# Kernel optimization log

Hardware: AMD Instinct MI355X
Metric: run time of the kernel (lower is better)

## Reference

```python
import jax, jax.numpy as jnp
import numpy as np

ANCHORS = np.array([[116.0, 90.0], [156.0, 198.0], [373.0, 326.0]], dtype=np.float32)
NUM_CLASSES = 80
IMG_DIM = 608.0
NA = 3  # num anchors


def setup_inputs() -> dict:
    key = jax.random.key(0)
    # raw head output: [B, nA*(nC+6), G, G]
    x = jax.random.normal(key, (32, NA * (NUM_CLASSES + 6), 76, 76), dtype=jnp.float32)
    return {"x": x}


def reference(x):
    B, _, G, _ = x.shape
    stride = IMG_DIM / G
    # [B, A, G, G, nC+6]
    pred = x.reshape(B, NA, NUM_CLASSES + 6, G, G).transpose(0, 1, 3, 4, 2)
    px = jax.nn.sigmoid(pred[..., 0])
    py = jax.nn.sigmoid(pred[..., 1])
    pw = pred[..., 2]
    ph = pred[..., 3]
    pconf = jax.nn.sigmoid(pred[..., 4])
    pcls = jax.nn.sigmoid(pred[..., 5:])  # nC+1 channels (iou_aware=False path)

    grid_x = jnp.arange(G, dtype=x.dtype)[None, None, None, :]  # varies along last (i) axis
    grid_y = jnp.arange(G, dtype=x.dtype)[None, None, :, None]  # varies along row (j) axis
    scaled_anchors = jnp.asarray(ANCHORS, dtype=x.dtype) / stride
    anchor_w = scaled_anchors[:, 0].reshape(1, NA, 1, 1)
    anchor_h = scaled_anchors[:, 1].reshape(1, NA, 1, 1)

    pred_boxes = jnp.stack(
        [px + grid_x, py + grid_y, jnp.exp(pw) * anchor_w, jnp.exp(ph) * anchor_h],
        axis=-1,
    )  # [B, A, G, G, 4]

    n = NA * G * G
    out = jnp.concatenate(
        [
            pred_boxes.reshape(B, n, 4) * stride,
            pconf.reshape(B, n, 1),
            pcls.reshape(B, n, -1),
        ],
        axis=-1,
    )  # [B, nA*G*G, 4+1+(nC+1)]
    return out
```

## Files before the change

kernel.cpp:

```cpp
#include <hip/hip_runtime.h>
#include <cstdint>


#define GDIM 76
#define SP   (GDIM * GDIM)
#define NCH  86
#define NANC 3
#define TS   64
#define NV   (NCH * TS / 4)

typedef float v4f __attribute__((ext_vector_type(4)));

__global__ __launch_bounds__(256) void yolo_decode_kernel(
    const float* __restrict__ in, float* __restrict__ out) {
    __shared__ __align__(16) float tile[TS * NCH];

    const int tid   = threadIdx.x;
    const int chunk = blockIdx.x;
    const int a     = blockIdx.y;
    const int b     = blockIdx.z;
    const int s0    = chunk * TS;
    const int valid = min(TS, SP - s0);

    const float aw = (a == 0) ? 116.0f : (a == 1) ? 156.0f : 373.0f;
    const float ah = (a == 0) ?  90.0f : (a == 1) ? 198.0f : 326.0f;

    const float* inp = in + ((size_t)(b * (NANC * NCH) + a * NCH)) * SP + s0;

    v4f vbuf[6];
    #pragma unroll
    for (int k = 0; k < 6; ++k) {
        const int idx = tid + (k << 8);
        const int c   = idx >> 4;
        const int s4  = (idx & 15) << 2;
        if (idx < NV && s4 < valid)
            vbuf[k] = *(const v4f*)(inp + (size_t)c * SP + s4);
    }

    #pragma unroll
    for (int k = 0; k < 6; ++k) {
        const int idx = tid + (k << 8);
        const int c   = idx >> 4;
        const int s4  = (idx & 15) << 2;
        if (idx < NV && s4 < valid) {
            v4f v = vbuf[k];
            if (c >= 4) {
                #pragma unroll
                for (int j = 0; j < 4; ++j)
                    v[j] = __builtin_amdgcn_rcpf(1.0f + __expf(-v[j]));
            } else if (c == 0) {
                const int sp_ = s0 + s4;
                #pragma unroll
                for (int j = 0; j < 4; ++j) {
                    const float sg = __builtin_amdgcn_rcpf(1.0f + __expf(-v[j]));
                    v[j] = (sg + (float)((sp_ + j) % GDIM)) * 8.0f;
                }
            } else if (c == 1) {
                const int sp_ = s0 + s4;
                #pragma unroll
                for (int j = 0; j < 4; ++j) {
                    const float sg = __builtin_amdgcn_rcpf(1.0f + __expf(-v[j]));
                    v[j] = (sg + (float)((sp_ + j) / GDIM)) * 8.0f;
                }
            } else {
                const float an = (c == 2) ? aw : ah;
                #pragma unroll
                for (int j = 0; j < 4; ++j)
                    v[j] = __expf(v[j]) * an;
            }
            #pragma unroll
            for (int j = 0; j < 4; ++j)
                tile[(s4 + j) * NCH + c] = v[j];
        }
    }
    __syncthreads();

    v4f* outp = (v4f*)(out + ((size_t)b * (NANC * SP) + (size_t)a * SP + (size_t)s0) * NCH);
    const int nvalid = (valid * NCH) >> 2;
    const v4f* lv = (const v4f*)tile;
    #pragma unroll
    for (int k = 0; k < 6; ++k) {
        const int v = tid + (k << 8);
        if (v < nvalid)
            __builtin_nontemporal_store(lv[v], outp + v);
    }
}

extern "C" void kernel_launch(void* const* d_in, const int* in_sizes, int n_in,
                              void* d_out, int out_size, void* d_ws, size_t ws_size,
                              hipStream_t stream) {
    const float* in = (const float*)d_in[0];
    float* out = (float*)d_out;
    const int B = in_sizes[0] / (NANC * NCH * SP);
    dim3 grid((SP + TS - 1) / TS, NANC, B);
    yolo_decode_kernel<<<grid, 256, 0, stream>>>(in, out);
}
```

Before: 322.5 us.

## Replace LDS transpose with per-thread channel loop writing output rows directly

Removes the shared-memory tile and barrier: each thread handles one spatial location, loads its 86 channels in four register batches, decodes them and writes its 86-float output row with 8-byte stores. This is meant to cut LDS traffic and synchronisation and to allow higher occupancy. In exchange, output stores within a wavefront become strided by the row size instead of contiguous, which risks poor write coalescing, and the nontemporal stores are dropped.

```diff
diff --git a/kernel.cpp b/kernel.cpp
--- a/kernel.cpp
+++ b/kernel.cpp
@@ -6,84 +6,61 @@
 #define SP   (GDIM * GDIM)
 #define NCH  86
 #define NANC 3
-#define TS   64
-#define NV   (NCH * TS / 4)
+#define TPB  256
 
-typedef float v4f __attribute__((ext_vector_type(4)));
+typedef float v2f __attribute__((ext_vector_type(2)));
 
-__global__ __launch_bounds__(256) void yolo_decode_kernel(
+__device__ __forceinline__ float fsig(float x) {
+    return __builtin_amdgcn_rcpf(1.0f + __expf(-x));
+}
+
+template<int C0, int NC>
+__device__ __forceinline__ void decode_pass(
+    const float* __restrict__ inp, float* __restrict__ orow,
+    float gx, float gy, float aw, float ah) {
+    float r[NC];
+    #pragma unroll
+    for (int i = 0; i < NC; ++i)
+        r[i] = inp[(size_t)(C0 + i) * SP];
+    #pragma unroll
+    for (int i = 0; i < NC; ++i) {
+        const int c = C0 + i;
+        const float x = r[i];
+        if      (c == 0) r[i] = (fsig(x) + gx) * 8.0f;
+        else if (c == 1) r[i] = (fsig(x) + gy) * 8.0f;
+        else if (c == 2) r[i] = __expf(x) * aw;
+        else if (c == 3) r[i] = __expf(x) * ah;
+        else             r[i] = fsig(x);
+    }
+    #pragma unroll
+    for (int p = 0; p < NC / 2; ++p) {
+        v2f t;
+        t.x = r[2 * p];
+        t.y = r[2 * p + 1];
+        *(v2f*)(orow + C0 + 2 * p) = t;
+    }
+}
+
+__global__ __launch_bounds__(TPB, 6) void yolo_decode_kernel(
     const float* __restrict__ in, float* __restrict__ out) {
-    __shared__ __align__(16) float tile[TS * NCH];
-
-    const int tid   = threadIdx.x;
-    const int chunk = blockIdx.x;
-    const int a     = blockIdx.y;
-    const int b     = blockIdx.z;
-    const int s0    = chunk * TS;
-    const int valid = min(TS, SP - s0);
+    const int s = blockIdx.x * TPB + threadIdx.x;
+    const int a = blockIdx.y;
+    const int b = blockIdx.z;
+    if (s >= SP) return;
 
     const float aw = (a == 0) ? 116.0f : (a == 1) ? 156.0f : 373.0f;
     const float ah = (a == 0) ?  90.0f : (a == 1) ? 198.0f : 326.0f;
 
-    const float* inp = in + ((size_t)(b * (NANC * NCH) + a * NCH)) * SP + s0;
+    const float* inp = in + (size_t)((b * NANC + a) * NCH) * SP + s;
+    float* orow = out + ((size_t)(b * NANC + a) * SP + (size_t)s) * NCH;
 
-    v4f vbuf[6];
-    #pragma unroll
-    for (int k = 0; k < 6; ++k) {
-        const int idx = tid + (k << 8);
-        const int c   = idx >> 4;
-        const int s4  = (idx & 15) << 2;
-        if (idx < NV && s4 < valid)
-            vbuf[k] = *(const v4f*)(inp + (size_t)c * SP + s4);
-    }
+    const float gx = (float)(s % GDIM);
+    const float gy = (float)(s / GDIM);
 
-    #pragma unroll
-    for (int k = 0; k < 6; ++k) {
-        const int idx = tid + (k << 8);
-        const int c   = idx >> 4;
-        const int s4  = (idx & 15) << 2;
-        if (idx < NV && s4 < valid) {
-            v4f v = vbuf[k];
-            if (c >= 4) {
-                #pragma unroll
-                for (int j = 0; j < 4; ++j)
-                    v[j] = __builtin_amdgcn_rcpf(1.0f + __expf(-v[j]));
-            } else if (c == 0) {
-                const int sp_ = s0 + s4;
-                #pragma unroll
-                for (int j = 0; j < 4; ++j) {
-                    const float sg = __builtin_amdgcn_rcpf(1.0f + __expf(-v[j]));
-                    v[j] = (sg + (float)((sp_ + j) % GDIM)) * 8.0f;
-                }
-            } else if (c == 1) {
-                const int sp_ = s0 + s4;
-                #pragma unroll
-                for (int j = 0; j < 4; ++j) {
-                    const float sg = __builtin_amdgcn_rcpf(1.0f + __expf(-v[j]));
-                    v[j] = (sg + (float)((sp_ + j) / GDIM)) * 8.0f;
-                }
-            } else {
-                const float an = (c == 2) ? aw : ah;
-                #pragma unroll
-                for (int j = 0; j < 4; ++j)
-                    v[j] = __expf(v[j]) * an;
-            }
-            #pragma unroll
-            for (int j = 0; j < 4; ++j)
-                tile[(s4 + j) * NCH + c] = v[j];
-        }
-    }
-    __syncthreads();
-
-    v4f* outp = (v4f*)(out + ((size_t)b * (NANC * SP) + (size_t)a * SP + (size_t)s0) * NCH);
-    const int nvalid = (valid * NCH) >> 2;
-    const v4f* lv = (const v4f*)tile;
-    #pragma unroll
-    for (int k = 0; k < 6; ++k) {
-        const int v = tid + (k << 8);
-        if (v < nvalid)
-            __builtin_nontemporal_store(lv[v], outp + v);
-    }
+    decode_pass< 0, 22>(inp, orow, gx, gy, aw, ah);
+    decode_pass<22, 22>(inp, orow, gx, gy, aw, ah);
+    decode_pass<44, 22>(inp, orow, gx, gy, aw, ah);
+    decode_pass<66, 20>(inp, orow, gx, gy, aw, ah);
 }
 
 extern "C" void kernel_launch(void* const* d_in, const int* in_sizes, int n_in,
@@ -92,6 +69,6 @@
     const float* in = (const float*)d_in[0];
     float* out = (float*)d_out;
     const int B = in_sizes[0] / (NANC * NCH * SP);
-    dim3 grid((SP + TS - 1) / TS, NANC, B);
-    yolo_decode_kernel<<<grid, 256, 0, stream>>>(in, out);
+    dim3 grid((SP + TPB - 1) / TPB, NANC, B);
+    yolo_decode_kernel<<<grid, TPB, 0, stream>>>(in, out);
 }
```

Result: slower. 404.7 us (+25.5%).

## Enlarge spatial tile to 256 with 1024-thread blocks and swizzled LDS transpose

Applied to the files above, without the earlier changes.

Raises the spatial tile from 64 to 256 positions per block and the block size from 256 to 1024 threads. Input reads per channel become 1 KB contiguous runs instead of 256 B. Adds an XOR swizzle on the LDS transpose buffer to cut bank conflicts on the scattered scalar writes, and replaces non-temporal output stores with regular stores. The tile now takes about 88 KB of LDS per block, which allows at most one block per CU. That limits occupancy and latency hiding, and the tail chunk is larger.

```diff
diff --git a/kernel.cpp b/kernel.cpp
--- a/kernel.cpp
+++ b/kernel.cpp
@@ -6,14 +6,24 @@
 #define SP   (GDIM * GDIM)
 #define NCH  86
 #define NANC 3
-#define TS   64
+#define TS   256
+#define TPB  1024
 #define NV   (NCH * TS / 4)
+#define NCHUNK ((SP + TS - 1) / TS)
 
 typedef float v4f __attribute__((ext_vector_type(4)));
 
-__global__ __launch_bounds__(256) void yolo_decode_kernel(
+__device__ __forceinline__ float fsig(float x) {
+    return __builtin_amdgcn_rcpf(1.0f + __expf(-x));
+}
+
+__device__ __forceinline__ int swz16(int byteoff) {
+    return byteoff ^ (((byteoff >> 9) & 7) << 4);
+}
+
+__global__ __launch_bounds__(TPB) void yolo_decode_kernel(
     const float* __restrict__ in, float* __restrict__ out) {
-    __shared__ __align__(16) float tile[TS * NCH];
+    __shared__ __align__(128) float tile[TS * NCH];
 
     const int tid   = threadIdx.x;
     const int chunk = blockIdx.x;
@@ -30,59 +40,54 @@
     v4f vbuf[6];
     #pragma unroll
     for (int k = 0; k < 6; ++k) {
-        const int idx = tid + (k << 8);
-        const int c   = idx >> 4;
-        const int s4  = (idx & 15) << 2;
+        const int idx = tid + k * TPB;
+        const int c   = idx >> 6;
+        const int s4  = (idx & 63) << 2;
         if (idx < NV && s4 < valid)
             vbuf[k] = *(const v4f*)(inp + (size_t)c * SP + s4);
     }
 
     #pragma unroll
     for (int k = 0; k < 6; ++k) {
-        const int idx = tid + (k << 8);
-        const int c   = idx >> 4;
-        const int s4  = (idx & 15) << 2;
+        const int idx = tid + k * TPB;
+        const int c   = idx >> 6;
+        const int s4  = (idx & 63) << 2;
         if (idx < NV && s4 < valid) {
             v4f v = vbuf[k];
             if (c >= 4) {
                 #pragma unroll
+                for (int j = 0; j < 4; ++j) v[j] = fsig(v[j]);
+            } else if (c == 0) {
+                #pragma unroll
                 for (int j = 0; j < 4; ++j)
-                    v[j] = __builtin_amdgcn_rcpf(1.0f + __expf(-v[j]));
-            } else if (c == 0) {
-                const int sp_ = s0 + s4;
+                    v[j] = (fsig(v[j]) + (float)((s0 + s4 + j) % GDIM)) * 8.0f;
+            } else if (c == 1) {
                 #pragma unroll
-                for (int j = 0; j < 4; ++j) {
-                    const float sg = __builtin_amdgcn_rcpf(1.0f + __expf(-v[j]));
-                    v[j] = (sg + (float)((sp_ + j) % GDIM)) * 8.0f;
-                }
-            } else if (c == 1) {
-                const int sp_ = s0 + s4;
-                #pragma unroll
-                for (int j = 0; j < 4; ++j) {
-                    const float sg = __builtin_amdgcn_rcpf(1.0f + __expf(-v[j]));
-                    v[j] = (sg + (float)((sp_ + j) / GDIM)) * 8.0f;
-                }
+                for (int j = 0; j < 4; ++j)
+                    v[j] = (fsig(v[j]) + (float)((s0 + s4 + j) / GDIM)) * 8.0f;
             } else {
                 const float an = (c == 2) ? aw : ah;
                 #pragma unroll
-                for (int j = 0; j < 4; ++j)
-                    v[j] = __expf(v[j]) * an;
+                for (int j = 0; j < 4; ++j) v[j] = __expf(v[j]) * an;
             }
             #pragma unroll
-            for (int j = 0; j < 4; ++j)
-                tile[(s4 + j) * NCH + c] = v[j];
+            for (int j = 0; j < 4; ++j) {
+                const int byteoff = ((s4 + j) * NCH + c) << 2;
+                *(float*)((char*)tile + swz16(byteoff)) = v[j];
+            }
         }
     }
     __syncthreads();
 
     v4f* outp = (v4f*)(out + ((size_t)b * (NANC * SP) + (size_t)a * SP + (size_t)s0) * NCH);
     const int nvalid = (valid * NCH) >> 2;
-    const v4f* lv = (const v4f*)tile;
     #pragma unroll
     for (int k = 0; k < 6; ++k) {
-        const int v = tid + (k << 8);
-        if (v < nvalid)
-            __builtin_nontemporal_store(lv[v], outp + v);
+        const int v = tid + k * TPB;
+        if (v < nvalid) {
+            const v4f t = *(const v4f*)((const char*)tile + swz16(v << 4));
+            outp[v] = t;
+        }
     }
 }
 
@@ -92,6 +97,6 @@
     const float* in = (const float*)d_in[0];
     float* out = (float*)d_out;
     const int B = in_sizes[0] / (NANC * NCH * SP);
-    dim3 grid((SP + TS - 1) / TS, NANC, B);
-    yolo_decode_kernel<<<grid, 256, 0, stream>>>(in, out);
+    dim3 grid(NCHUNK, NANC, B);
+    yolo_decode_kernel<<<grid, TPB, 0, stream>>>(in, out);
 }
```

Result: no change. 318.4 us (-1.3%).
